# Kernel tuning notes

Measured on AMD Instinct MI355X. Metric: run time of the kernel, lower is better.

Reference implementation:

```python
import jax, jax.numpy as jnp
import numpy as np

# ---- geometry constants (from init_kwargs) ----
VOL_SHAPE = (96, 96, 96)        # (Z, Y, X)
VOL_SPACING = 1.0               # mm, isotropic
N_PROJ = 180
DET_ROWS, DET_COLS = 192, 384   # (v, u)
DET_SPACING_V, DET_SPACING_U = 1.0, 1.0
SID = 750.0                     # source-isocenter distance
SDD = 1200.0                    # source-detector distance


def _proj_matrices():
    """3x4 pinhole projection matrices for a circular cone-beam trajectory."""
    cu = (DET_COLS - 1) / 2.0
    cv = (DET_ROWS - 1) / 2.0
    Kc = np.array([[SDD / DET_SPACING_U, 0.0, cu],
                   [0.0, SDD / DET_SPACING_V, cv],
                   [0.0, 0.0, 1.0]])
    mats = []
    for th in np.linspace(0.0, 2.0 * np.pi, N_PROJ, endpoint=False):
        s = SID * np.array([np.cos(th), np.sin(th), 0.0])   # source position
        ez = -s / SID                                        # optical axis -> isocenter
        ex = np.array([-np.sin(th), np.cos(th), 0.0])        # detector u axis
        ey = np.array([0.0, 0.0, 1.0])                       # detector v axis
        R = np.stack([ex, ey, ez])                           # world -> camera
        P = Kc @ np.concatenate([R, (-R @ s)[:, None]], axis=1)
        mats.append(P)
    return np.stack(mats).astype(np.float32)                # [P, 3, 4]


def _voxel_coords():
    """Homogeneous world coordinates of all voxel centers, [4, N]."""
    zs = (np.arange(VOL_SHAPE[0]) - (VOL_SHAPE[0] - 1) / 2.0) * VOL_SPACING
    ys = (np.arange(VOL_SHAPE[1]) - (VOL_SHAPE[1] - 1) / 2.0) * VOL_SPACING
    xs = (np.arange(VOL_SHAPE[2]) - (VOL_SHAPE[2] - 1) / 2.0) * VOL_SPACING
    Z, Y, X = np.meshgrid(zs, ys, xs, indexing='ij')
    pts = np.stack([X.ravel(), Y.ravel(), Z.ravel(), np.ones(X.size)])
    return pts.astype(np.float32)


def _bilinear(img, u, v):
    """Zero-padded bilinear interpolation of img[H,W] at (v,u) pixel coords."""
    H, W = img.shape
    u0 = jnp.floor(u); v0 = jnp.floor(v)
    fu = u - u0; fv = v - v0
    u0i = u0.astype(jnp.int32); v0i = v0.astype(jnp.int32)
    def at(vi, ui):
        valid = (ui >= 0) & (ui < W) & (vi >= 0) & (vi < H)
        val = img[jnp.clip(vi, 0, H - 1), jnp.clip(ui, 0, W - 1)]
        return jnp.where(valid, val, jnp.zeros((), img.dtype))
    return (at(v0i, u0i) * (1 - fu) * (1 - fv)
            + at(v0i, u0i + 1) * fu * (1 - fv)
            + at(v0i + 1, u0i) * (1 - fu) * fv
            + at(v0i + 1, u0i + 1) * fu * fv)


def _backproject_one(sino, mats, coords):
    """sino [P,H,W], mats [P,3,4], coords [4,N] -> volume [Z,Y,X]."""
    N = coords.shape[1]
    @jax.checkpoint
    def step(acc, pm_s):
        P, s = pm_s
        uvw = P @ coords                      # [3, N]
        w = uvw[2]                            # ray depth along optical axis (>0)
        u = uvw[0] / w
        v = uvw[1] / w
        acc = acc + _bilinear(s, u, v) / (w * w)  # FDK distance weighting
        return acc, None
    acc, _ = jax.lax.scan(step, jnp.zeros((N,), sino.dtype), (mats, sino))
    return acc.reshape(VOL_SHAPE)


def setup_inputs() -> dict:
    key = jax.random.key(0)
    x = jax.random.normal(key, (2, N_PROJ, DET_ROWS, DET_COLS, 1), dtype=jnp.float32)
    proj_matrices = jnp.asarray(_proj_matrices())
    return {"x": x, "proj_matrices": proj_matrices}


def reference(x, proj_matrices):
    coords = jnp.asarray(_voxel_coords())                 # [4, N]
    sinos = jnp.squeeze(x, -1)                            # [B, P, H, W]
    vols = jax.vmap(lambda s: _backproject_one(s, proj_matrices, coords))(sinos)
    return vols[..., None]                                # [B, Z, Y, X, 1]
```

## Files before the change

kernel.cpp:

```cpp
#include <hip/hip_runtime.h>

#define NPROJ 180
#define PHALF 90
#define DH 192
#define DW 384
#define VN 96
#define ZPER 4
#define TCOLS 65
#define TROWS 14
#define TENT (TCOLS * TROWS)
#define TPAD 1024
#define PSTRIDE (DH * DW)
#define BSTRIDE (NPROJ * DH * DW)

typedef float v2f __attribute__((ext_vector_type(2)));

__global__ __launch_bounds__(256, 6) void cone_bp(
    const float* __restrict__ sino,
    const float* __restrict__ mats,
    float* __restrict__ out)
{
    __shared__ v2f tile[2][TPAD];
    __shared__ int2 anch[PHALF];

    const int tid = threadIdx.x;
    const int x = blockIdx.x * 32 + ((tid & 7) | ((tid >> 6) << 3));
    const int y = blockIdx.y * 8 + ((tid >> 3) & 7);
    const int half = (blockIdx.z >= 24) ? 1 : 0;
    const int zc = blockIdx.z - 24 * half;
    const int pbase = half * PHALF;

    const float xw = (float)x - 47.5f;
    const float yw = (float)y - 47.5f;
    const float zw0 = (float)(zc * ZPER) - 47.5f;

    const float xwc = (float)(blockIdx.x * 32) - 32.0f;
    const float ywc = (float)(blockIdx.y * 8) - 44.0f;
    const float zwc = (float)(zc * ZPER) - 46.0f;

    const float4* __restrict__ M = (const float4*)mats;

    if (tid < PHALF) {
        int p = pbase + tid;
        float4 a0 = M[p * 3 + 0];
        float4 a1 = M[p * 3 + 1];
        float4 a2 = M[p * 3 + 2];
        float unc = fmaf(a0.x, xwc, fmaf(a0.y, ywc, a0.w));
        float vnc = fmaf(a1.x, xwc, fmaf(a1.y, ywc, fmaf(a1.z, zwc, a1.w)));
        float wc  = fmaf(a2.x, xwc, fmaf(a2.y, ywc, a2.w));
        float rwc = __builtin_amdgcn_rcpf(wc);
        anch[tid] = make_int2((int)floorf(unc * rwc) - 31,
                              (int)floorf(vnc * rwc) - 6);
    }

    int VgB[4];
#pragma unroll
    for (int k = 0; k < 4; ++k) {
        int li = tid + 256 * k;
        int row = li / TCOLS;
        int col = li - row * TCOLS;
        VgB[k] = (row * DW + col) * 4;
    }

    __syncthreads();

    int cu, cv;
    {
        int2 a = anch[0];
        cu = __builtin_amdgcn_readfirstlane(a.x);
        cv = __builtin_amdgcn_readfirstlane(a.y);
    }
    v2f g[4];
    {
        const char* p0 = (const char*)(sino + pbase * PSTRIDE + cv * DW + cu);
        const char* p1 = p0 + (size_t)BSTRIDE * 4;
#pragma unroll
        for (int k = 0; k < 4; ++k) {
            g[k].x = *(const float*)(p0 + VgB[k]);
            g[k].y = *(const float*)(p1 + VgB[k]);
        }
    }

    v2f acc[ZPER];
#pragma unroll
    for (int k = 0; k < ZPER; ++k) acc[k] = (v2f)(0.0f);

    auto body = [&](int i, v2f* __restrict__ buf) {
#pragma unroll
        for (int k = 0; k < 4; ++k)
            buf[tid + 256 * k] = g[k];
        const float nfu = -(float)cu;
        const float nfv = -(float)cv;

        if (i + 1 < PHALF) {
            int2 a = anch[i + 1];
            cu = __builtin_amdgcn_readfirstlane(a.x);
            cv = __builtin_amdgcn_readfirstlane(a.y);
            const char* p0 = (const char*)(sino
                + (pbase + i + 1) * PSTRIDE + cv * DW + cu);
            const char* p1 = p0 + (size_t)BSTRIDE * 4;
#pragma unroll
            for (int k = 0; k < 4; ++k) {
                g[k].x = *(const float*)(p0 + VgB[k]);
                g[k].y = *(const float*)(p1 + VgB[k]);
            }
        }

        __syncthreads();

        const int p = pbase + i;
        float4 r0 = M[p * 3 + 0];
        float4 r1 = M[p * 3 + 1];
        float4 r2 = M[p * 3 + 2];
        float un  = fmaf(r0.x, xw, fmaf(r0.y, yw, r0.w));
        float vn0 = fmaf(r1.x, xw, fmaf(r1.y, yw, r1.w));
        float w   = fmaf(r2.x, xw, fmaf(r2.y, yw, r2.w));
        float rw  = __builtin_amdgcn_rcpf(w);
        float iw2 = rw * rw;
        float ul  = fmaf(un, rw, nfu);
        float uf  = floorf(ul);
        float fu  = ul - uf;
        int   u0l = (int)uf;
        float vb  = fmaf(fmaf(r1.z, zw0, vn0), rw, nfv);
        float dv  = r1.z * rw;

        int   o[ZPER];
        float fv[ZPER];
#pragma unroll
        for (int k = 0; k < ZPER; ++k) {
            float v  = fmaf(dv, (float)k, vb);
            float vf = floorf(v);
            fv[k] = v - vf;
            o[k] = (int)vf * TCOLS + u0l;
        }
        v2f E00[ZPER], E01[ZPER], E10[ZPER], E11[ZPER];
#pragma unroll
        for (int k = 0; k < ZPER; ++k) {
            E00[k] = buf[o[k]];
            E01[k] = buf[o[k] + 1];
            E10[k] = buf[o[k] + TCOLS];
            E11[k] = buf[o[k] + TCOLS + 1];
        }
#pragma unroll
        for (int k = 0; k < ZPER; ++k) {
            v2f F0 = E00[k] + (E10[k] - E00[k]) * fv[k];
            v2f F1 = E01[k] + (E11[k] - E01[k]) * fv[k];
            v2f H  = F0 + (F1 - F0) * fu;
            acc[k] += H * iw2;
        }
    };

    for (int i = 0; i < PHALF; i += 2) {
        body(i,     tile[0]);
        body(i + 1, tile[1]);
    }

    const int zbase = zc * ZPER;
#pragma unroll
    for (int k = 0; k < ZPER; ++k) {
        unsafeAtomicAdd(&out[(((size_t)(zbase + k)) * VN + y) * VN + x],
                        acc[k].x);
        unsafeAtomicAdd(&out[(((size_t)(VN + zbase + k)) * VN + y) * VN + x],
                        acc[k].y);
    }
}

extern "C" void kernel_launch(void* const* d_in, const int* in_sizes, int n_in,
                              void* d_out, int out_size, void* d_ws, size_t ws_size,
                              hipStream_t stream) {
    const float* sino = (const float*)d_in[0];
    const float* mats = (const float*)d_in[1];
    float* out = (float*)d_out;

    hipMemsetAsync(out, 0, (size_t)out_size * sizeof(float), stream);

    dim3 grid(VN / 32, VN / 8, 48), block(256);
    hipLaunchKernelGGL(cone_bp, grid, block, 0, stream, sino, mats, out);
}
```

Baseline: 290.0 us.

## Process eight z-slices per block and split projections into quarters with workspace

Each block now accumulates 8 z-slices instead of 4 from a taller staged detector tile (19 rows), so each loaded tile feeds twice the voxels. To keep enough blocks in flight, the projection range is split into four quarters instead of two. Atomics from half of those quarters go to a zeroed workspace buffer, which a separate kernel adds into the output, spreading atomic contention across two buffers. The changes add an extra memset and kernel launch, more registers and shared memory per block, and a larger tile that may not cover every footprint.

```diff
diff --git a/kernel.cpp b/kernel.cpp
--- a/kernel.cpp
+++ b/kernel.cpp
@@ -1,34 +1,35 @@
 #include <hip/hip_runtime.h>
 
 #define NPROJ 180
-#define PHALF 90
 #define DH 192
 #define DW 384
 #define VN 96
-#define ZPER 4
+#define ZPER 8
+#define ZCH (VN / ZPER)
 #define TCOLS 65
-#define TROWS 14
-#define TENT (TCOLS * TROWS)
-#define TPAD 1024
+#define TROWS 19
+#define TSTG 1280
 #define PSTRIDE (DH * DW)
 #define BSTRIDE (NPROJ * DH * DW)
 
 typedef float v2f __attribute__((ext_vector_type(2)));
 
+template<int PQ, int NQ>
 __global__ __launch_bounds__(256, 6) void cone_bp(
     const float* __restrict__ sino,
     const float* __restrict__ mats,
-    float* __restrict__ out)
+    float* __restrict__ out,
+    float* __restrict__ ws)
 {
-    __shared__ v2f tile[2][TPAD];
-    __shared__ int2 anch[PHALF];
+    __shared__ v2f tile[2][TSTG];
+    __shared__ int2 anch[PQ];
 
     const int tid = threadIdx.x;
     const int x = blockIdx.x * 32 + ((tid & 7) | ((tid >> 6) << 3));
     const int y = blockIdx.y * 8 + ((tid >> 3) & 7);
-    const int half = (blockIdx.z >= 24) ? 1 : 0;
-    const int zc = blockIdx.z - 24 * half;
-    const int pbase = half * PHALF;
+    const int zc = blockIdx.z % ZCH;
+    const int qt = blockIdx.z / ZCH;
+    const int pbase = qt * PQ;
 
     const float xw = (float)x - 47.5f;
     const float yw = (float)y - 47.5f;
@@ -36,11 +37,11 @@
 
     const float xwc = (float)(blockIdx.x * 32) - 32.0f;
     const float ywc = (float)(blockIdx.y * 8) - 44.0f;
-    const float zwc = (float)(zc * ZPER) - 46.0f;
+    const float zwc = (float)(zc * ZPER) - 44.0f;
 
     const float4* __restrict__ M = (const float4*)mats;
 
-    if (tid < PHALF) {
+    if (tid < PQ) {
         int p = pbase + tid;
         float4 a0 = M[p * 3 + 0];
         float4 a1 = M[p * 3 + 1];
@@ -50,12 +51,12 @@
         float wc  = fmaf(a2.x, xwc, fmaf(a2.y, ywc, a2.w));
         float rwc = __builtin_amdgcn_rcpf(wc);
         anch[tid] = make_int2((int)floorf(unc * rwc) - 31,
-                              (int)floorf(vnc * rwc) - 6);
-    }
-
-    int VgB[4];
-#pragma unroll
-    for (int k = 0; k < 4; ++k) {
+                              (int)floorf(vnc * rwc) - 9);
+    }
+
+    int VgB[5];
+#pragma unroll
+    for (int k = 0; k < 5; ++k) {
         int li = tid + 256 * k;
         int row = li / TCOLS;
         int col = li - row * TCOLS;
@@ -70,12 +71,12 @@
         cu = __builtin_amdgcn_readfirstlane(a.x);
         cv = __builtin_amdgcn_readfirstlane(a.y);
     }
-    v2f g[4];
+    v2f g[5];
     {
         const char* p0 = (const char*)(sino + pbase * PSTRIDE + cv * DW + cu);
         const char* p1 = p0 + (size_t)BSTRIDE * 4;
 #pragma unroll
-        for (int k = 0; k < 4; ++k) {
+        for (int k = 0; k < 5; ++k) {
             g[k].x = *(const float*)(p0 + VgB[k]);
             g[k].y = *(const float*)(p1 + VgB[k]);
         }
@@ -87,12 +88,12 @@
 
     auto body = [&](int i, v2f* __restrict__ buf) {
 #pragma unroll
-        for (int k = 0; k < 4; ++k)
+        for (int k = 0; k < 5; ++k)
             buf[tid + 256 * k] = g[k];
         const float nfu = -(float)cu;
         const float nfv = -(float)cv;
 
-        if (i + 1 < PHALF) {
+        if (i + 1 < PQ) {
             int2 a = anch[i + 1];
             cu = __builtin_amdgcn_readfirstlane(a.x);
             cv = __builtin_amdgcn_readfirstlane(a.y);
@@ -100,7 +101,7 @@
                 + (pbase + i + 1) * PSTRIDE + cv * DW + cu);
             const char* p1 = p0 + (size_t)BSTRIDE * 4;
 #pragma unroll
-            for (int k = 0; k < 4; ++k) {
+            for (int k = 0; k < 5; ++k) {
                 g[k].x = *(const float*)(p0 + VgB[k]);
                 g[k].y = *(const float*)(p1 + VgB[k]);
             }
@@ -124,44 +125,60 @@
         float vb  = fmaf(fmaf(r1.z, zw0, vn0), rw, nfv);
         float dv  = r1.z * rw;
 
-        int   o[ZPER];
-        float fv[ZPER];
-#pragma unroll
-        for (int k = 0; k < ZPER; ++k) {
-            float v  = fmaf(dv, (float)k, vb);
-            float vf = floorf(v);
-            fv[k] = v - vf;
-            o[k] = (int)vf * TCOLS + u0l;
-        }
-        v2f E00[ZPER], E01[ZPER], E10[ZPER], E11[ZPER];
-#pragma unroll
-        for (int k = 0; k < ZPER; ++k) {
-            E00[k] = buf[o[k]];
-            E01[k] = buf[o[k] + 1];
-            E10[k] = buf[o[k] + TCOLS];
-            E11[k] = buf[o[k] + TCOLS + 1];
-        }
-#pragma unroll
-        for (int k = 0; k < ZPER; ++k) {
-            v2f F0 = E00[k] + (E10[k] - E00[k]) * fv[k];
-            v2f F1 = E01[k] + (E11[k] - E01[k]) * fv[k];
-            v2f H  = F0 + (F1 - F0) * fu;
-            acc[k] += H * iw2;
+#pragma unroll
+        for (int gz = 0; gz < 2; ++gz) {
+            int   o[4];
+            float fv[4];
+#pragma unroll
+            for (int j = 0; j < 4; ++j) {
+                float v  = fmaf(dv, (float)(4 * gz + j), vb);
+                float vf = floorf(v);
+                fv[j] = v - vf;
+                o[j] = (int)vf * TCOLS + u0l;
+            }
+            v2f E00[4], E01[4], E10[4], E11[4];
+#pragma unroll
+            for (int j = 0; j < 4; ++j) {
+                E00[j] = buf[o[j]];
+                E01[j] = buf[o[j] + 1];
+                E10[j] = buf[o[j] + TCOLS];
+                E11[j] = buf[o[j] + TCOLS + 1];
+            }
+#pragma unroll
+            for (int j = 0; j < 4; ++j) {
+                v2f F0 = E00[j] + (E10[j] - E00[j]) * fv[j];
+                v2f F1 = E01[j] + (E11[j] - E01[j]) * fv[j];
+                v2f H  = F0 + (F1 - F0) * fu;
+                acc[4 * gz + j] += H * iw2;
+            }
         }
     };
 
-    for (int i = 0; i < PHALF; i += 2) {
-        body(i,     tile[0]);
-        body(i + 1, tile[1]);
-    }
-
+    for (int i = 0; i < PQ; i += 2) {
+        body(i, tile[0]);
+        if (i + 1 < PQ) body(i + 1, tile[1]);
+    }
+
+    float* __restrict__ dst = (NQ == 4 && qt >= 2) ? ws : out;
     const int zbase = zc * ZPER;
 #pragma unroll
     for (int k = 0; k < ZPER; ++k) {
-        unsafeAtomicAdd(&out[(((size_t)(zbase + k)) * VN + y) * VN + x],
+        unsafeAtomicAdd(&dst[(((size_t)(zbase + k)) * VN + y) * VN + x],
                         acc[k].x);
-        unsafeAtomicAdd(&out[(((size_t)(VN + zbase + k)) * VN + y) * VN + x],
+        unsafeAtomicAdd(&dst[(((size_t)(VN + zbase + k)) * VN + y) * VN + x],
                         acc[k].y);
+    }
+}
+
+__global__ __launch_bounds__(256) void add_ws(
+    float4* __restrict__ out, const float4* __restrict__ ws, int n4)
+{
+    int i = blockIdx.x * 256 + threadIdx.x;
+    if (i < n4) {
+        float4 a = ws[i];
+        float4 b = out[i];
+        b.x += a.x; b.y += a.y; b.z += a.z; b.w += a.w;
+        out[i] = b;
     }
 }
 
@@ -171,9 +188,22 @@
     const float* sino = (const float*)d_in[0];
     const float* mats = (const float*)d_in[1];
     float* out = (float*)d_out;
-
+    float* wsf = (float*)d_ws;
+
+    const size_t nvox = (size_t)2 * VN * VN * VN;
     hipMemsetAsync(out, 0, (size_t)out_size * sizeof(float), stream);
 
-    dim3 grid(VN / 32, VN / 8, 48), block(256);
-    hipLaunchKernelGGL(cone_bp, grid, block, 0, stream, sino, mats, out);
+    if (ws_size >= nvox * sizeof(float)) {
+        hipMemsetAsync(wsf, 0, nvox * sizeof(float), stream);
+        dim3 grid(VN / 32, VN / 8, ZCH * 4), block(256);
+        hipLaunchKernelGGL((cone_bp<NPROJ / 4, 4>), grid, block, 0, stream,
+                           sino, mats, out, wsf);
+        int n4 = (int)(nvox / 4);
+        hipLaunchKernelGGL(add_ws, dim3((n4 + 255) / 256), block, 0, stream,
+                           (float4*)out, (const float4*)wsf, n4);
+    } else {
+        dim3 grid(VN / 32, VN / 8, ZCH * 2), block(256);
+        hipLaunchKernelGGL((cone_bp<NPROJ / 2, 2>), grid, block, 0, stream,
+                           sino, mats, out, (float*)nullptr);
+    }
 }
```

After: 311.4 us. 7.4% more time.

## Deepen global prefetch to two projections ahead with custom LDS-only barrier

Applied to the files above, without the earlier changes.

The sinogram tile prefetch now keeps two register sets in flight, loading projection i+2 and i+3 while i and i+1 are sampled, so each global load has about two iterations of latency to hide. The __syncthreads is replaced by an inline-asm barrier that waits only on LDS counters (lgkmcnt) and not on outstanding vector memory loads. This lets global loads stay in flight across the barrier. The cost is doubled prefetch registers, which may hurt occupancy at the 6-wave launch bound.

```diff
diff --git a/kernel.cpp b/kernel.cpp
--- a/kernel.cpp
+++ b/kernel.cpp
@@ -8,12 +8,13 @@
 #define ZPER 4
 #define TCOLS 65
 #define TROWS 14
-#define TENT (TCOLS * TROWS)
 #define TPAD 1024
 #define PSTRIDE (DH * DW)
 #define BSTRIDE (NPROJ * DH * DW)
 
 typedef float v2f __attribute__((ext_vector_type(2)));
+
+#define BAR() asm volatile("s_waitcnt lgkmcnt(0)\n\ts_barrier" ::: "memory")
 
 __global__ __launch_bounds__(256, 6) void cone_bp(
     const float* __restrict__ sino,
@@ -64,50 +65,38 @@
 
     __syncthreads();
 
-    int cu, cv;
-    {
-        int2 a = anch[0];
-        cu = __builtin_amdgcn_readfirstlane(a.x);
-        cv = __builtin_amdgcn_readfirstlane(a.y);
-    }
-    v2f g[4];
-    {
-        const char* p0 = (const char*)(sino + pbase * PSTRIDE + cv * DW + cu);
+    auto issue = [&](int p, int cu, int cv, v2f* g) {
+        const char* p0 = (const char*)(sino + (size_t)p * PSTRIDE + cv * DW + cu);
         const char* p1 = p0 + (size_t)BSTRIDE * 4;
 #pragma unroll
         for (int k = 0; k < 4; ++k) {
             g[k].x = *(const float*)(p0 + VgB[k]);
             g[k].y = *(const float*)(p1 + VgB[k]);
         }
+    };
+
+    int cu, cv;
+    v2f gA[4], gB[4];
+    {
+        int2 a = anch[0];
+        cu = __builtin_amdgcn_readfirstlane(a.x);
+        cv = __builtin_amdgcn_readfirstlane(a.y);
     }
+    issue(pbase, cu, cv, gA);
+    float nfuA = -(float)cu, nfvA = -(float)cv;
+    {
+        int2 a = anch[1];
+        cu = __builtin_amdgcn_readfirstlane(a.x);
+        cv = __builtin_amdgcn_readfirstlane(a.y);
+    }
+    issue(pbase + 1, cu, cv, gB);
+    float nfuB = -(float)cu, nfvB = -(float)cv;
 
     v2f acc[ZPER];
 #pragma unroll
     for (int k = 0; k < ZPER; ++k) acc[k] = (v2f)(0.0f);
 
-    auto body = [&](int i, v2f* __restrict__ buf) {
-#pragma unroll
-        for (int k = 0; k < 4; ++k)
-            buf[tid + 256 * k] = g[k];
-        const float nfu = -(float)cu;
-        const float nfv = -(float)cv;
-
-        if (i + 1 < PHALF) {
-            int2 a = anch[i + 1];
-            cu = __builtin_amdgcn_readfirstlane(a.x);
-            cv = __builtin_amdgcn_readfirstlane(a.y);
-            const char* p0 = (const char*)(sino
-                + (pbase + i + 1) * PSTRIDE + cv * DW + cu);
-            const char* p1 = p0 + (size_t)BSTRIDE * 4;
-#pragma unroll
-            for (int k = 0; k < 4; ++k) {
-                g[k].x = *(const float*)(p0 + VgB[k]);
-                g[k].y = *(const float*)(p1 + VgB[k]);
-            }
-        }
-
-        __syncthreads();
-
+    auto sample = [&](int i, const v2f* buf, float nfu, float nfv) {
         const int p = pbase + i;
         float4 r0 = M[p * 3 + 0];
         float4 r1 = M[p * 3 + 1];
@@ -151,8 +140,36 @@
     };
 
     for (int i = 0; i < PHALF; i += 2) {
-        body(i,     tile[0]);
-        body(i + 1, tile[1]);
+        {
+#pragma unroll
+            for (int k = 0; k < 4; ++k)
+                tile[0][tid + 256 * k] = gA[k];
+            const float su = nfuA, sv = nfvA;
+            if (i + 2 < PHALF) {
+                int2 a = anch[i + 2];
+                cu = __builtin_amdgcn_readfirstlane(a.x);
+                cv = __builtin_amdgcn_readfirstlane(a.y);
+                issue(pbase + i + 2, cu, cv, gA);
+                nfuA = -(float)cu; nfvA = -(float)cv;
+            }
+            BAR();
+            sample(i, tile[0], su, sv);
+        }
+        {
+#pragma unroll
+            for (int k = 0; k < 4; ++k)
+                tile[1][tid + 256 * k] = gB[k];
+            const float su = nfuB, sv = nfvB;
+            if (i + 3 < PHALF) {
+                int2 a = anch[i + 3];
+                cu = __builtin_amdgcn_readfirstlane(a.x);
+                cv = __builtin_amdgcn_readfirstlane(a.y);
+                issue(pbase + i + 3, cu, cv, gB);
+                nfuB = -(float)cu; nfvB = -(float)cv;
+            }
+            BAR();
+            sample(i + 1, tile[1], su, sv);
+        }
     }
 
     const int zbase = zc * ZPER;
```

Result: slower. 605.3 us (+108.7%).
